# Kernel optimization log

Measured on AMD Instinct MI355X. Metric: run time of the kernel, lower is better.

Reference implementation:

```python
import jax, jax.numpy as jnp
import numpy as np

SIZE, DIM, BATCH, K = 131072, 128, 1024, 16


def _l2_normalize(x, axis):
    return x / jnp.linalg.norm(x, axis=axis, keepdims=True)


def setup_inputs() -> dict:
    key = jax.random.key(0)
    k1, k2, k3, k4, k5 = jax.random.split(key, 5)
    # bank init as in MemoryBank._create: uniform in [-std, std], then l2-normalized rows
    std = 1.0 / np.sqrt(DIM / 3)
    bank = jax.random.uniform(k1, (SIZE, DIM), dtype=jnp.float32) * (2 * std) - std
    bank = _l2_normalize(bank, 1)
    emb_batch = _l2_normalize(jax.random.normal(k2, (BATCH, DIM), dtype=jnp.float32), 1)
    data_memory = _l2_normalize(jax.random.normal(k3, (BATCH, DIM), dtype=jnp.float32), 1)
    idxs = jax.random.randint(k4, (BATCH, K), 0, SIZE)
    update_indices = jax.random.randint(k5, (BATCH,), 0, SIZE)
    return {
        "emb_batch": emb_batch,
        "data_memory": data_memory,
        "bank": bank,
        "idxs": idxs,
        "update_indices": update_indices,
    }


def reference(emb_batch, data_memory, bank, idxs, update_indices):
    # get_all_dot_products: [B, S]
    all_dots = jnp.matmul(emb_batch, bank.T)
    # get_all_distances: ||b_j - e_i||. Original materializes [B,S,D] differences;
    # mathematically identical expansion avoids the huge intermediate.
    e_sq = jnp.sum(emb_batch * emb_batch, axis=1)[:, None]   # [B,1]
    b_sq = jnp.sum(bank * bank, axis=1)[None, :]             # [1,S]
    distances = jnp.sqrt(jnp.maximum(e_sq + b_sq - 2.0 * all_dots, 0.0))  # [B,S]
    # get_dot_products with 2D idxs: gather [B,K,D] then multiply-sum -> [B,K]
    knn_dots = jnp.einsum("bkd,bd->bk", bank[idxs], emb_batch)
    # update: scatter rows of data_memory into the bank
    new_bank = bank.at[update_indices].set(data_memory)
    return distances, all_dots, knn_dots, new_bank
```

## Files before the change

kernel.cpp:

```cpp
#include <hip/hip_runtime.h>
#include <hip/hip_bf16.h>

typedef __bf16 bf16x8 __attribute__((ext_vector_type(8)));
typedef float  f32x4  __attribute__((ext_vector_type(4)));

#define SIZE_  131072
#define DIM_   128
#define BATCH_ 1024
#define KNN_   16

#define BM 64
#define BN 64
#define MT (BATCH_ / BM)
#define NT (SIZE_ / BN)
#define NWG (MT * NT)

__global__ __launch_bounds__(256) void prep_emb(const float* __restrict__ emb,
                                                __bf16* __restrict__ emb16,
                                                float* __restrict__ e_sq) {
    int wid  = (blockIdx.x * 256 + threadIdx.x) >> 6;
    int lane = threadIdx.x & 63;
    float2 v = *reinterpret_cast<const float2*>(emb + (size_t)wid * DIM_ + lane * 2);
    float s = v.x * v.x + v.y * v.y;
    #pragma unroll
    for (int off = 32; off; off >>= 1) s += __shfl_xor(s, off);
    union { __bf16 h[2]; unsigned int u; } pk;
    pk.h[0] = (__bf16)v.x; pk.h[1] = (__bf16)v.y;
    *reinterpret_cast<unsigned int*>(emb16 + (size_t)wid * DIM_ + lane * 2) = pk.u;
    if (lane == 0) e_sq[wid] = s;
}

__global__ __launch_bounds__(256) void gemm_dist(const float* __restrict__ bank,
                                                 const __bf16* __restrict__ emb16,
                                                 const float* __restrict__ e_sq,
                                                 const float* __restrict__ emb,
                                                 const int* __restrict__ idxs,
                                                 float* __restrict__ out_dist,
                                                 float* __restrict__ out_dots,
                                                 float* __restrict__ out_bank,
                                                 float* __restrict__ out_knn) {
    __shared__ alignas(16) char smem[33024];
    char*  lBc   = smem;
    char*  ftile = smem;
    float* bsq   = (float*)(smem + 32768);

    int bid  = blockIdx.x;
    int tid  = threadIdx.x;
    int wv   = tid >> 6;
    int lane = tid & 63;

    if (bid < (BATCH_ * KNN_) / 4) {
        int wid = bid * 4 + wv;
        int b   = wid >> 4;
        int idx = idxs[wid];
        float2 br = *reinterpret_cast<const float2*>(bank + (size_t)idx * DIM_ + lane * 2);
        float2 er = *reinterpret_cast<const float2*>(emb + (size_t)b * DIM_ + lane * 2);
        float s = br.x * er.x + br.y * er.y;
        #pragma unroll
        for (int off = 32; off; off >>= 1) s += __shfl_xor(s, off);
        if (lane == 0) out_knn[wid] = s;
    }

    int logical = (bid & 7) * (NWG / 8) + (bid >> 3);
    int mt = logical & (MT - 1);
    int nt = logical >> 4;
    int m0 = mt * BM;
    int n0 = nt * BN;

    int lr   = lane & 15;
    int rgrp = lane >> 4;
    int lkb  = rgrp * 8;

    bf16x8 af[4];
    {
        const __bf16* abase = emb16 + (size_t)(m0 + wv * 16 + lr) * DIM_ + lkb;
        #pragma unroll
        for (int ks = 0; ks < 4; ++ks)
            af[ks] = *reinterpret_cast<const bf16x8*>(abase + ks * 32);
    }

    #pragma unroll
    for (int i = 0; i < 4; ++i) {
        int p   = i * 256 + tid;
        int row = p >> 4;
        int k0  = (p & 15) * 8;
        size_t gb = (size_t)(n0 + row) * DIM_ + k0;
        const f32x4* s4 = reinterpret_cast<const f32x4*>(bank + gb);
        f32x4 a = s4[0], b = s4[1];
        if (mt == 0) {
            __builtin_nontemporal_store(a, reinterpret_cast<f32x4*>(out_bank + gb));
            __builtin_nontemporal_store(b, reinterpret_cast<f32x4*>(out_bank + gb + 4));
        }
        float s = a.x * a.x + a.y * a.y + a.z * a.z + a.w * a.w
                + b.x * b.x + b.y * b.y + b.z * b.z + b.w * b.w;
        #pragma unroll
        for (int off = 8; off; off >>= 1) s += __shfl_xor(s, off);
        if ((p & 15) == 0) bsq[row] = s;
        union { __bf16 h[8]; int4 v; } pk;
        pk.h[0] = (__bf16)a.x; pk.h[1] = (__bf16)a.y; pk.h[2] = (__bf16)a.z; pk.h[3] = (__bf16)a.w;
        pk.h[4] = (__bf16)b.x; pk.h[5] = (__bf16)b.y; pk.h[6] = (__bf16)b.z; pk.h[7] = (__bf16)b.w;
        int o  = (row << 8) + k0 * 2;
        int so = o ^ ((row & 7) << 4);
        *reinterpret_cast<int4*>(lBc + so) = pk.v;
    }
    __syncthreads();

    f32x4 acc[4] = {};
    #pragma unroll
    for (int ks = 0; ks < 4; ++ks) {
        int kk = ks * 32 + lkb;
        bf16x8 bf[4];
        #pragma unroll
        for (int nc = 0; nc < 4; ++nc) {
            int row = nc * 16 + lr;
            int o   = (row << 8) + kk * 2;
            bf[nc]  = *reinterpret_cast<const bf16x8*>(lBc + (o ^ ((row & 7) << 4)));
        }
        #pragma unroll
        for (int nc = 0; nc < 4; ++nc)
            acc[nc] = __builtin_amdgcn_mfma_f32_16x16x32_bf16(af[ks], bf[nc], acc[nc], 0, 0, 0);
    }

    float bs[4];
    #pragma unroll
    for (int nc = 0; nc < 4; ++nc) bs[nc] = bsq[nc * 16 + lr];
    float es[4];
    #pragma unroll
    for (int j = 0; j < 4; ++j) es[j] = e_sq[m0 + wv * 16 + rgrp * 4 + j];

    __syncthreads();

    #pragma unroll
    for (int j = 0; j < 4; ++j) {
        int row = wv * 16 + rgrp * 4 + j;
        int sw  = (row & 7) << 4;
        #pragma unroll
        for (int nc = 0; nc < 4; ++nc) {
            float d   = acc[nc][j];
            float arg = es[j] + bs[nc] - 2.0f * d;
            int o = (row << 8) + (nc * 16 + lr) * 4;
            *reinterpret_cast<float*>(ftile + (o ^ sw))         = sqrtf(fmaxf(arg, 0.0f));
            *reinterpret_cast<float*>(ftile + 16384 + (o ^ sw)) = d;
        }
    }
    __syncthreads();

    #pragma unroll
    for (int i = 0; i < 8; ++i) {
        int p    = i * 256 + tid;
        int half = p >> 10;
        int pr   = p & 1023;
        int row  = pr >> 4;
        int c4   = pr & 15;
        int o    = (row << 8) + c4 * 16;
        f32x4 v = *reinterpret_cast<const f32x4*>(ftile + half * 16384 + (o ^ ((row & 7) << 4)));
        size_t ga = (size_t)(m0 + row) * SIZE_ + n0 + c4 * 4;
        float* outp = half ? out_dots : out_dist;
        __builtin_nontemporal_store(v, reinterpret_cast<f32x4*>(outp + ga));
    }
}

__global__ __launch_bounds__(128) void scatter_rows(const float* __restrict__ dmem,
                                                    const int* __restrict__ upd,
                                                    float* __restrict__ newbank) {
    int i = blockIdx.x;
    int idx = upd[i];
    __shared__ int dup;
    if (threadIdx.x == 0) dup = 0;
    __syncthreads();
    for (int j = i + 1 + threadIdx.x; j < BATCH_; j += 128)
        if (upd[j] == idx) dup = 1;
    __syncthreads();
    if (dup) return;
    newbank[(size_t)idx * DIM_ + threadIdx.x] = dmem[(size_t)i * DIM_ + threadIdx.x];
}

extern "C" void kernel_launch(void* const* d_in, const int* in_sizes, int n_in,
                              void* d_out, int out_size, void* d_ws, size_t ws_size,
                              hipStream_t stream) {
    const float* emb  = (const float*)d_in[0];
    const float* dmem = (const float*)d_in[1];
    const float* bank = (const float*)d_in[2];
    const int*   idxs = (const int*)d_in[3];
    const int*   upd  = (const int*)d_in[4];

    float* out       = (float*)d_out;
    float* out_dist  = out;
    float* out_dots  = out + (size_t)BATCH_ * SIZE_;
    float* out_knn   = out + (size_t)2 * BATCH_ * SIZE_;
    float* out_bank  = out_knn + (size_t)BATCH_ * KNN_;

    char*   ws    = (char*)d_ws;
    float*  e_sq  = (float*)ws;
    __bf16* emb16 = (__bf16*)(ws + 4096);

    prep_emb <<<BATCH_ / 4, 256, 0, stream>>>(emb, emb16, e_sq);
    gemm_dist<<<NWG,        256, 0, stream>>>(bank, emb16, e_sq, emb, idxs,
                                              out_dist, out_dots, out_bank, out_knn);
    scatter_rows<<<BATCH_,  128, 0, stream>>>(dmem, upd, out_bank);
}
```

Baseline: 258.9 us.

## Widen GEMM N-tile to 256 columns with per-64 sub-tile loop and chunked epilogue

Each workgroup now covers 256 bank rows instead of 64. It loops over four 64-row sub-tiles, reusing the A fragments held in registers and keeping 16 accumulators per lane. The epilogue writes 128-column chunks through LDS so that stores to the output rows are 512 bytes contiguous. The intent is to cut the number of workgroups, the per-workgroup A loads and launch overhead, and to improve write coalescing. In exchange it adds register pressure, more __syncthreads barriers, and less parallelism from fewer blocks.

```diff
diff --git a/kernel.cpp b/kernel.cpp
--- a/kernel.cpp
+++ b/kernel.cpp
@@ -10,7 +10,7 @@
 #define KNN_   16
 
 #define BM 64
-#define BN 64
+#define BN 256
 #define MT (BATCH_ / BM)
 #define NT (SIZE_ / BN)
 #define NWG (MT * NT)
@@ -39,7 +39,7 @@
                                                  float* __restrict__ out_dots,
                                                  float* __restrict__ out_bank,
                                                  float* __restrict__ out_knn) {
-    __shared__ alignas(16) char smem[33024];
+    __shared__ alignas(16) char smem[33792];
     char*  lBc   = smem;
     char*  ftile = smem;
     float* bsq   = (float*)(smem + 32768);
@@ -79,84 +79,90 @@
             af[ks] = *reinterpret_cast<const bf16x8*>(abase + ks * 32);
     }
 
-    #pragma unroll
-    for (int i = 0; i < 4; ++i) {
-        int p   = i * 256 + tid;
-        int row = p >> 4;
-        int k0  = (p & 15) * 8;
-        size_t gb = (size_t)(n0 + row) * DIM_ + k0;
-        const f32x4* s4 = reinterpret_cast<const f32x4*>(bank + gb);
-        f32x4 a = s4[0], b = s4[1];
-        if (mt == 0) {
-            __builtin_nontemporal_store(a, reinterpret_cast<f32x4*>(out_bank + gb));
-            __builtin_nontemporal_store(b, reinterpret_cast<f32x4*>(out_bank + gb + 4));
-        }
-        float s = a.x * a.x + a.y * a.y + a.z * a.z + a.w * a.w
-                + b.x * b.x + b.y * b.y + b.z * b.z + b.w * b.w;
-        #pragma unroll
-        for (int off = 8; off; off >>= 1) s += __shfl_xor(s, off);
-        if ((p & 15) == 0) bsq[row] = s;
-        union { __bf16 h[8]; int4 v; } pk;
-        pk.h[0] = (__bf16)a.x; pk.h[1] = (__bf16)a.y; pk.h[2] = (__bf16)a.z; pk.h[3] = (__bf16)a.w;
-        pk.h[4] = (__bf16)b.x; pk.h[5] = (__bf16)b.y; pk.h[6] = (__bf16)b.z; pk.h[7] = (__bf16)b.w;
-        int o  = (row << 8) + k0 * 2;
-        int so = o ^ ((row & 7) << 4);
-        *reinterpret_cast<int4*>(lBc + so) = pk.v;
-    }
-    __syncthreads();
-
-    f32x4 acc[4] = {};
-    #pragma unroll
-    for (int ks = 0; ks < 4; ++ks) {
-        int kk = ks * 32 + lkb;
-        bf16x8 bf[4];
-        #pragma unroll
-        for (int nc = 0; nc < 4; ++nc) {
-            int row = nc * 16 + lr;
-            int o   = (row << 8) + kk * 2;
-            bf[nc]  = *reinterpret_cast<const bf16x8*>(lBc + (o ^ ((row & 7) << 4)));
-        }
-        #pragma unroll
-        for (int nc = 0; nc < 4; ++nc)
-            acc[nc] = __builtin_amdgcn_mfma_f32_16x16x32_bf16(af[ks], bf[nc], acc[nc], 0, 0, 0);
-    }
-
-    float bs[4];
-    #pragma unroll
-    for (int nc = 0; nc < 4; ++nc) bs[nc] = bsq[nc * 16 + lr];
+    f32x4 acc[16] = {};
+
+    #pragma unroll
+    for (int r = 0; r < 4; ++r) {
+        int nr0 = n0 + r * 64;
+        #pragma unroll
+        for (int i = 0; i < 4; ++i) {
+            int p   = i * 256 + tid;
+            int row = p >> 4;
+            int k0  = (p & 15) * 8;
+            size_t gb = (size_t)(nr0 + row) * DIM_ + k0;
+            const f32x4* s4 = reinterpret_cast<const f32x4*>(bank + gb);
+            f32x4 a = s4[0], b = s4[1];
+            if (mt == 0) {
+                __builtin_nontemporal_store(a, reinterpret_cast<f32x4*>(out_bank + gb));
+                __builtin_nontemporal_store(b, reinterpret_cast<f32x4*>(out_bank + gb + 4));
+            }
+            float s = a.x * a.x + a.y * a.y + a.z * a.z + a.w * a.w
+                    + b.x * b.x + b.y * b.y + b.z * b.z + b.w * b.w;
+            #pragma unroll
+            for (int off = 8; off; off >>= 1) s += __shfl_xor(s, off);
+            if ((p & 15) == 0) bsq[r * 64 + row] = s;
+            union { __bf16 h[8]; int4 v; } pk;
+            pk.h[0] = (__bf16)a.x; pk.h[1] = (__bf16)a.y; pk.h[2] = (__bf16)a.z; pk.h[3] = (__bf16)a.w;
+            pk.h[4] = (__bf16)b.x; pk.h[5] = (__bf16)b.y; pk.h[6] = (__bf16)b.z; pk.h[7] = (__bf16)b.w;
+            int o  = (row << 8) + k0 * 2;
+            int so = o ^ ((row & 7) << 4);
+            *reinterpret_cast<int4*>(lBc + so) = pk.v;
+        }
+        __syncthreads();
+
+        #pragma unroll
+        for (int ks = 0; ks < 4; ++ks) {
+            int kk = ks * 32 + lkb;
+            bf16x8 bf[4];
+            #pragma unroll
+            for (int nc = 0; nc < 4; ++nc) {
+                int row = nc * 16 + lr;
+                int o   = (row << 8) + kk * 2;
+                bf[nc]  = *reinterpret_cast<const bf16x8*>(lBc + (o ^ ((row & 7) << 4)));
+            }
+            #pragma unroll
+            for (int nc = 0; nc < 4; ++nc)
+                acc[r * 4 + nc] = __builtin_amdgcn_mfma_f32_16x16x32_bf16(af[ks], bf[nc], acc[r * 4 + nc], 0, 0, 0);
+        }
+        __syncthreads();
+    }
+
+    float bsv[16];
+    #pragma unroll
+    for (int a = 0; a < 16; ++a) bsv[a] = bsq[a * 16 + lr];
     float es[4];
     #pragma unroll
     for (int j = 0; j < 4; ++j) es[j] = e_sq[m0 + wv * 16 + rgrp * 4 + j];
 
-    __syncthreads();
-
-    #pragma unroll
-    for (int j = 0; j < 4; ++j) {
-        int row = wv * 16 + rgrp * 4 + j;
-        int sw  = (row & 7) << 4;
-        #pragma unroll
-        for (int nc = 0; nc < 4; ++nc) {
-            float d   = acc[nc][j];
-            float arg = es[j] + bs[nc] - 2.0f * d;
-            int o = (row << 8) + (nc * 16 + lr) * 4;
-            *reinterpret_cast<float*>(ftile + (o ^ sw))         = sqrtf(fmaxf(arg, 0.0f));
-            *reinterpret_cast<float*>(ftile + 16384 + (o ^ sw)) = d;
-        }
-    }
-    __syncthreads();
-
-    #pragma unroll
-    for (int i = 0; i < 8; ++i) {
-        int p    = i * 256 + tid;
-        int half = p >> 10;
-        int pr   = p & 1023;
-        int row  = pr >> 4;
-        int c4   = pr & 15;
-        int o    = (row << 8) + c4 * 16;
-        f32x4 v = *reinterpret_cast<const f32x4*>(ftile + half * 16384 + (o ^ ((row & 7) << 4)));
-        size_t ga = (size_t)(m0 + row) * SIZE_ + n0 + c4 * 4;
+    #pragma unroll
+    for (int h = 0; h < 4; ++h) {
+        int half = h >> 1;
+        int ch   = h & 1;
+        #pragma unroll
+        for (int a8 = 0; a8 < 8; ++a8) {
+            int a = ch * 8 + a8;
+            #pragma unroll
+            for (int j = 0; j < 4; ++j) {
+                int row = wv * 16 + rgrp * 4 + j;
+                float d = acc[a][j];
+                float val = half ? d : sqrtf(fmaxf(es[j] + bsv[a] - 2.0f * d, 0.0f));
+                int o = (row << 9) + (a8 * 16 + lr) * 4;
+                *reinterpret_cast<float*>(ftile + (o ^ ((row & 7) << 4))) = val;
+            }
+        }
+        __syncthreads();
         float* outp = half ? out_dots : out_dist;
-        __builtin_nontemporal_store(v, reinterpret_cast<f32x4*>(outp + ga));
+        #pragma unroll
+        for (int i = 0; i < 8; ++i) {
+            int p   = i * 256 + tid;
+            int row = p >> 5;
+            int c4  = p & 31;
+            int o   = (row << 9) + c4 * 16;
+            f32x4 v = *reinterpret_cast<const f32x4*>(ftile + (o ^ ((row & 7) << 4)));
+            size_t ga = (size_t)(m0 + row) * SIZE_ + n0 + ch * 128 + c4 * 4;
+            __builtin_nontemporal_store(v, reinterpret_cast<f32x4*>(outp + ga));
+        }
+        __syncthreads();
     }
 }
 
```

Result: slower. 338.1 us (+30.6%).
